# Optimization experiments

Hardware: AMD Instinct MI355X
Metric: run time of the kernel (lower is better)

## Reference

```python
import jax, jax.numpy as jnp
import numpy as np

N_CELL, N_NET, N_GCELL = 50000, 10000, 20000
E = 100000
D = 32   # hidden_node = hidden_net = hidden_hanna = out_node = out_net
DP = 16  # hidden_pin = hidden_edge feats


def setup_inputs() -> dict:
    key = jax.random.key(0)
    ks = jax.random.split(key, 21)
    f = jax.random.normal
    ri = lambda k, n: jax.random.randint(k, (E,), 0, n, dtype=jnp.int32)
    return {
        'node_feat': f(ks[0], (N_CELL, D), jnp.float32),
        'net_feat': f(ks[1], (N_NET, D), jnp.float32),
        'pin_feat': f(ks[2], (E, DP), jnp.float32),
        'hanna_feat': f(ks[3], (N_GCELL, D), jnp.float32),
        'edge_feat': f(ks[4], (E, DP), jnp.float32),
        'pins_src': ri(ks[5], N_CELL), 'pins_dst': ri(ks[6], N_NET),
        'pinned_src': ri(ks[7], N_NET), 'pinned_dst': ri(ks[8], N_CELL),
        'connect_src': ri(ks[9], N_GCELL), 'connect_dst': ri(ks[10], N_GCELL),
        'pt_src': ri(ks[11], N_CELL), 'pt_dst': ri(ks[12], N_GCELL),
        'pf_src': ri(ks[13], N_GCELL), 'pf_dst': ri(ks[14], N_CELL),
        'W_net': f(ks[15], (D, D)) * 0.1, 'b_net': jnp.zeros((D,), jnp.float32),
        'W_topo': f(ks[16], (DP, D * D)) * 0.1, 'b_topo': jnp.zeros((D * D,), jnp.float32),
        'W_pins': f(ks[17], (D, D)) * 0.1, 'b_pins': jnp.zeros((D,), jnp.float32),
        'W_connect': f(ks[18], (D, D)) * 0.1, 'b_connect': jnp.zeros((D,), jnp.float32),
        'W_pt': f(ks[19], (D, D)) * 0.1, 'b_pt': jnp.zeros((D,), jnp.float32),
        'b_pinned': jnp.zeros((D,), jnp.float32), 'b_pf': jnp.zeros((D,), jnp.float32),
    }


def _deg(idx, n):
    # clamped degree, as DGL clamps to min 1
    return jnp.maximum(jax.ops.segment_sum(jnp.ones_like(idx, jnp.float32), idx, n), 1.0)


def graph_conv(h_src, W, b, src, dst, n_src, n_dst):
    # DGL GraphConv with norm='both': D_out^{-1/2} gather -> sum -> D_in^{-1/2}, then W, b
    feat = (h_src * _deg(src, n_src)[:, None] ** -0.5) @ W
    agg = jax.ops.segment_sum(feat[src], dst, n_dst)
    return agg * _deg(dst, n_dst)[:, None] ** -0.5 + b


def nn_conv(h_src, efeat, W_topo, b_topo, bias, src, dst, n_dst):
    # DGL NNConv (aggregator='mean'): per-edge weight from edge_func, mean over in-edges
    d_in = h_src.shape[1]
    w = (efeat @ W_topo + b_topo).reshape(-1, d_in, bias.shape[0])  # (E, d_in, d_out)
    m = jnp.einsum('ei,eio->eo', h_src[src], w)
    return jax.ops.segment_sum(m, dst, n_dst) / _deg(dst, n_dst)[:, None] + bias


def reference(node_feat, net_feat, pin_feat, hanna_feat, edge_feat,
              pins_src, pins_dst, pinned_src, pinned_dst, connect_src, connect_dst,
              pt_src, pt_dst, pf_src, pf_dst,
              W_net, b_net, W_topo, b_topo, W_pins, b_pins,
              W_connect, b_connect, W_pt, b_pt, b_pinned, b_pf):
    # 'pins': cell -> net (GraphConv)
    h_net = graph_conv(node_feat, W_pins, b_pins, pins_src, pins_dst, N_CELL, N_NET)
    # 'pinned': net -> cell (NNConv) + 'point-from': gcell -> cell (NNConv); agg='sum'
    h_cell = (nn_conv(net_feat, pin_feat, W_topo, b_topo, b_pinned, pinned_src, pinned_dst, N_CELL)
              + nn_conv(hanna_feat, edge_feat, W_topo, b_topo, b_pf, pf_src, pf_dst, N_CELL))
    # 'connect': gcell -> gcell + 'point-to': cell -> gcell (GraphConvs); agg='sum'
    h_gcell = (graph_conv(hanna_feat, W_connect, b_connect, connect_src, connect_dst, N_GCELL, N_GCELL)
               + graph_conv(node_feat, W_pt, b_pt, pt_src, pt_dst, N_CELL, N_GCELL))
    return (h_cell, h_net + net_feat @ W_net + b_net, h_gcell)
```

## Files before the change

kernel.cpp:

```cpp
#include <hip/hip_runtime.h>

typedef unsigned short u16;
typedef unsigned int u32;

#define NC 50000
#define NN 10000
#define NG 20000
#define NE 100000
#define NSCAN 150016
#define NBLK 74


__device__ __forceinline__ float bflo(u32 a) { return __uint_as_float(a << 16); }
__device__ __forceinline__ float bfhi(u32 a) { return __uint_as_float(a & 0xFFFF0000u); }
__device__ __forceinline__ u16 fbf(float f) {
  u32 u = __float_as_uint(f);
  return (u16)((u + 0x7FFFu + ((u >> 16) & 1u)) >> 16);
}

__device__ __forceinline__ float nn_msg(int e, int s, const float* __restrict__ ef,
                                        const u16* __restrict__ T,
                                        const float* __restrict__ C, int o) {
  const float4* efp = reinterpret_cast<const float4*>(ef + (size_t)e * 16);
  float4 ea = efp[0], eb = efp[1], ec = efp[2], ed = efp[3];
  const uint4* tp = reinterpret_cast<const uint4*>(T + (size_t)s * 512 + o * 16);
  uint4 ta = tp[0], tb = tp[1];
  float m = C[(size_t)s * 32 + o];
  m += ea.x * bflo(ta.x) + ea.y * bfhi(ta.x) + ea.z * bflo(ta.y) + ea.w * bfhi(ta.y);
  m += eb.x * bflo(ta.z) + eb.y * bfhi(ta.z) + eb.z * bflo(ta.w) + eb.w * bfhi(ta.w);
  m += ec.x * bflo(tb.x) + ec.y * bfhi(tb.x) + ec.z * bflo(tb.y) + ec.w * bfhi(tb.y);
  m += ed.x * bflo(tb.z) + ed.y * bfhi(tb.z) + ed.z * bflo(tb.w) + ed.w * bfhi(tb.w);
  return m;
}

__global__ __launch_bounds__(512) void k_front(
    const float* __restrict__ feat_net, const float* __restrict__ feat_han,
    const float* __restrict__ W_topo, const float* __restrict__ b_topo,
    u16* __restrict__ T_net, u16* __restrict__ T_han,
    float* __restrict__ C_net, float* __restrict__ C_han,
    const int* __restrict__ pins_src, const int* __restrict__ pins_dst,
    const int* __restrict__ pinned_dst, const int* __restrict__ pf_dst,
    const int* __restrict__ connect_src, const int* __restrict__ connect_dst,
    const int* __restrict__ pt_src, const int* __restrict__ pt_dst,
    int* __restrict__ hist, int* __restrict__ srccnt) {
  int b = blockIdx.x;
  int tid = threadIdx.x;
  if (b < 469) {
    __shared__ float hs[64][32];
    int nd0 = b * 64;
    {
      int idx = tid * 4;
      int nl = idx >> 5, i = idx & 31;
      int ng = nd0 + nl;
      int ngc = min(ng, 29999);
      const float* rp = (ngc < NN) ? feat_net + (size_t)ngc * 32
                                   : feat_han + (size_t)(ngc - NN) * 32;
      *reinterpret_cast<float4*>(&hs[nl][i]) =
          *reinterpret_cast<const float4*>(rp + i);
    }
    int jj = tid & 255;
    int j0 = jj * 2, j1 = j0 + 1;
    int p0 = j0 & 15, o0 = j0 >> 4;
    int p1 = j1 & 15, o1 = j1 >> 4;
    float w0[32], w1[32];
#pragma unroll
    for (int i = 0; i < 32; i++) {
      w0[i] = W_topo[p0 * 1024 + i * 32 + o0];
      w1[i] = W_topo[p1 * 1024 + i * 32 + o1];
    }
    __syncthreads();
    int g = tid >> 8;
#pragma unroll 4
    for (int n = 0; n < 32; n++) {
      int nl = g * 32 + n;
      float a0 = 0.f, a1 = 0.f;
#pragma unroll
      for (int i = 0; i < 32; i++) {
        float h = hs[nl][i];
        a0 += h * w0[i];
        a1 += h * w1[i];
      }
      int s = nd0 + nl;
      if (s < 30000) {
        u32 pk = (u32)fbf(a0) | ((u32)fbf(a1) << 16);
        u32* dst = (s < NN)
            ? reinterpret_cast<u32*>(T_net + (size_t)s * 512 + j0)
            : reinterpret_cast<u32*>(T_han + (size_t)(s - NN) * 512 + j0);
        *dst = pk;
      }
    }
    return;
  }
  if (b < 2344) {
    int t = (b - 469) * 512 + tid;
    int s2 = t >> 5, o = t & 31;
    bool han = s2 >= NN;
    const float* feat = han ? feat_han : feat_net;
    float* C = han ? C_han : C_net;
    int s = han ? s2 - NN : s2;
    float acc = 0.f;
#pragma unroll 8
    for (int i = 0; i < 32; i++)
      acc += feat[(size_t)s * 32 + i] * b_topo[i * 32 + o];
    C[(size_t)s * 32 + o] = acc;
    return;
  }
  int e = (b - 2344) * 512 + tid;
  if (e >= NE) return;
  atomicAdd(&hist[pins_dst[e]], 1);
  atomicAdd(&hist[10000 + connect_dst[e]], 1);
  atomicAdd(&hist[30000 + pt_dst[e]], 1);
  atomicAdd(&hist[50000 + pinned_dst[e]], 1);
  atomicAdd(&hist[100000 + pf_dst[e]], 1);
  atomicAdd(&srccnt[pins_src[e]], 1);
  atomicAdd(&srccnt[50000 + connect_src[e]], 1);
  atomicAdd(&srccnt[70000 + pt_src[e]], 1);
}

__global__ __launch_bounds__(256) void k_scan1(
    const int* __restrict__ cnt, int* __restrict__ bsum) {
  __shared__ int sm[256];
  int b = blockIdx.x, tid = threadIdx.x;
  int base = b * 2048 + tid * 8;
  int tot = 0;
#pragma unroll
  for (int j = 0; j < 8; j++) {
    int i = base + j;
    tot += (i < NSCAN) ? cnt[i] : 0;
  }
  sm[tid] = tot;
  __syncthreads();
  for (int off = 128; off > 0; off >>= 1) {
    if (tid < off) sm[tid] += sm[tid + off];
    __syncthreads();
  }
  if (tid == 0) bsum[b] = sm[0];
}

__global__ __launch_bounds__(256) void k_scan3(
    const int* __restrict__ cnt, const int* __restrict__ bsum,
    int* __restrict__ bases) {
  __shared__ int sm[256];
  __shared__ int carry;
  int b = blockIdx.x, tid = threadIdx.x;
  if (tid == 0) {
    int run = 0;
    for (int i = 0; i < b; i++) run += bsum[i];
    carry = run;
  }
  int base = b * 2048 + tid * 8;
  int v[8];
  int tot = 0;
#pragma unroll
  for (int j = 0; j < 8; j++) {
    int i = base + j;
    v[j] = (i < NSCAN) ? cnt[i] : 0;
    tot += v[j];
  }
  sm[tid] = tot;
  __syncthreads();
  for (int off = 1; off < 256; off <<= 1) {
    int add = (tid >= off) ? sm[tid - off] : 0;
    __syncthreads();
    sm[tid] += add;
    __syncthreads();
  }
  int excl = sm[tid] - tot + carry;
#pragma unroll
  for (int j = 0; j < 8; j++) {
    int i = base + j;
    if (i < NSCAN) bases[i] = excl;
    excl += v[j];
  }
}

__global__ __launch_bounds__(512) void k_fill(
    const int* __restrict__ pins_src, const int* __restrict__ pins_dst,
    const int* __restrict__ connect_src, const int* __restrict__ connect_dst,
    const int* __restrict__ pt_src, const int* __restrict__ pt_dst,
    const int* __restrict__ pinned_src, const int* __restrict__ pinned_dst,
    const int* __restrict__ pf_src, const int* __restrict__ pf_dst,
    const int* __restrict__ srccnt,
    const int* __restrict__ bases, int* __restrict__ cursor,
    int2* __restrict__ csr_gc, int2* __restrict__ csr_nn) {
  int t = blockIdx.x * 512 + threadIdx.x;
  if (t >= 5 * NE) return;
  int r = (t >= NE) + (t >= 2 * NE) + (t >= 3 * NE) + (t >= 4 * NE);
  int e = t - r * NE;
  const int* srcs = r == 0 ? pins_src : r == 1 ? connect_src
                   : r == 2 ? pt_src : r == 3 ? pinned_src : pf_src;
  const int* dsts = r == 0 ? pins_dst : r == 1 ? connect_dst
                   : r == 2 ? pt_dst : r == 3 ? pinned_dst : pf_dst;
  int off = r == 0 ? 0 : r == 1 ? 10000 : r == 2 ? 30000 : r == 3 ? 50000 : 100000;
  int s = srcs[e];
  int g = off + dsts[e];
  int pos = atomicAdd(&cursor[g], 1);
  int cpos = bases[g] + pos;
  if (r < 3) {
    int soff = r == 0 ? 0 : r == 1 ? 50000 : 70000;
    float w = rsqrtf(fmaxf((float)srccnt[soff + s], 1.f));
    csr_gc[cpos] = make_int2(s, __float_as_int(w));
  } else {
    csr_nn[cpos - 300000] = make_int2(e, s);
  }
}

__global__ __launch_bounds__(512) void k_gc_gather(
    const int* __restrict__ hist, const int* __restrict__ bases,
    const int2* __restrict__ csr_gc,
    const float* __restrict__ node_feat, const float* __restrict__ hanna_feat,
    float* __restrict__ S_net, float* __restrict__ S_conn, float* __restrict__ S_pt) {
  int t = blockIdx.x * 512 + threadIdx.x;
  int rr = t >> 5, o = t & 31;
  int rel = (rr >= 10000) + (rr >= 30000);
  const float* feat = (rel == 1) ? hanna_feat : node_feat;
  float* S = rel == 0 ? S_net + (size_t)rr * 32
           : rel == 1 ? S_conn + (size_t)(rr - 10000) * 32
                      : S_pt + (size_t)(rr - 30000) * 32;
  int base = bases[rr], deg = hist[rr];
  float acc = 0.f;
  int k = 0;
  for (; k + 1 < deg; k += 2) {
    int2 pa = csr_gc[base + k], pb = csr_gc[base + k + 1];
    acc += feat[(size_t)pa.x * 32 + o] * __int_as_float(pa.y) +
           feat[(size_t)pb.x * 32 + o] * __int_as_float(pb.y);
  }
  if (k < deg) {
    int2 pa = csr_gc[base + k];
    acc += feat[(size_t)pa.x * 32 + o] * __int_as_float(pa.y);
  }
  S[o] = acc;
}

__global__ __launch_bounds__(512) void k_tail(
    const int* __restrict__ hist, const int* __restrict__ bases,
    const int2* __restrict__ csr_nn,
    const float* __restrict__ pin_feat, const float* __restrict__ edge_feat,
    const u16* __restrict__ T_net, const u16* __restrict__ T_han,
    const float* __restrict__ C_net, const float* __restrict__ C_han,
    const float* __restrict__ b_pinned, const float* __restrict__ b_pf,
    const float* __restrict__ S_net, const float* __restrict__ net_feat,
    const float* __restrict__ W_pins, const float* __restrict__ b_pins,
    const float* __restrict__ W_net, const float* __restrict__ b_net,
    const float* __restrict__ S_conn, const float* __restrict__ S_pt,
    const float* __restrict__ W_connect, const float* __restrict__ b_connect,
    const float* __restrict__ W_pt, const float* __restrict__ b_pt,
    float* __restrict__ out) {
  __shared__ float Wa[1024], Wb[1024];
  int b = blockIdx.x;
  if (b < 3125) {
    int t = b * 512 + threadIdx.x;
    int d = t >> 5, o = t & 31;
    float a0 = 0.f, a1 = 0.f;
    {
      int g = 50000 + d;
      int base = bases[g] - 300000, deg = hist[g];
      int k = 0;
      for (; k + 1 < deg; k += 2) {
        int2 ea = csr_nn[base + k], eb = csr_nn[base + k + 1];
        a0 += nn_msg(ea.x, ea.y, pin_feat, T_net, C_net, o) +
              nn_msg(eb.x, eb.y, pin_feat, T_net, C_net, o);
      }
      if (k < deg) {
        int2 ea = csr_nn[base + k];
        a0 += nn_msg(ea.x, ea.y, pin_feat, T_net, C_net, o);
      }
      a0 /= fmaxf((float)deg, 1.f);
    }
    {
      int g = 100000 + d;
      int base = bases[g] - 300000, deg = hist[g];
      int k = 0;
      for (; k + 1 < deg; k += 2) {
        int2 ea = csr_nn[base + k], eb = csr_nn[base + k + 1];
        a1 += nn_msg(ea.x, ea.y, edge_feat, T_han, C_han, o) +
              nn_msg(eb.x, eb.y, edge_feat, T_han, C_han, o);
      }
      if (k < deg) {
        int2 ea = csr_nn[base + k];
        a1 += nn_msg(ea.x, ea.y, edge_feat, T_han, C_han, o);
      }
      a1 /= fmaxf((float)deg, 1.f);
    }
    out[(size_t)d * 32 + o] = a0 + a1 + b_pinned[o] + b_pf[o];
    return;
  }
  if (b < 3750) {
    for (int k = threadIdx.x; k < 1024; k += 512) {
      Wa[k] = W_pins[k];
      Wb[k] = W_net[k];
    }
    __syncthreads();
    int t = (b - 3125) * 512 + threadIdx.x;
    int r = t >> 5, o = t & 31;
    float a1 = 0.f, a2 = 0.f;
#pragma unroll 8
    for (int i = 0; i < 32; i++) {
      a1 += S_net[(size_t)r * 32 + i] * Wa[i * 32 + o];
      a2 += net_feat[(size_t)r * 32 + i] * Wb[i * 32 + o];
    }
    out[1600000 + t] = a1 * rsqrtf(fmaxf((float)hist[r], 1.f)) + b_pins[o] +
                       a2 + b_net[o];
    return;
  }
  for (int k = threadIdx.x; k < 1024; k += 512) {
    Wa[k] = W_connect[k];
    Wb[k] = W_pt[k];
  }
  __syncthreads();
  int t = (b - 3750) * 512 + threadIdx.x;
  int r = t >> 5, o = t & 31;
  float a1 = 0.f, a2 = 0.f;
#pragma unroll 8
  for (int i = 0; i < 32; i++) {
    a1 += S_conn[(size_t)r * 32 + i] * Wa[i * 32 + o];
    a2 += S_pt[(size_t)r * 32 + i] * Wb[i * 32 + o];
  }
  out[1920000 + t] = a1 * rsqrtf(fmaxf((float)hist[10000 + r], 1.f)) + b_connect[o] +
                     a2 * rsqrtf(fmaxf((float)hist[30000 + r], 1.f)) + b_pt[o];
}

extern "C" void kernel_launch(void* const* d_in, const int* in_sizes, int n_in,
                              void* d_out, int out_size, void* d_ws, size_t ws_size,
                              hipStream_t stream) {
  const float* node_feat  = (const float*)d_in[0];
  const float* net_feat   = (const float*)d_in[1];
  const float* pin_feat   = (const float*)d_in[2];
  const float* hanna_feat = (const float*)d_in[3];
  const float* edge_feat  = (const float*)d_in[4];
  const int* pins_src    = (const int*)d_in[5];
  const int* pins_dst    = (const int*)d_in[6];
  const int* pinned_src  = (const int*)d_in[7];
  const int* pinned_dst  = (const int*)d_in[8];
  const int* connect_src = (const int*)d_in[9];
  const int* connect_dst = (const int*)d_in[10];
  const int* pt_src      = (const int*)d_in[11];
  const int* pt_dst      = (const int*)d_in[12];
  const int* pf_src      = (const int*)d_in[13];
  const int* pf_dst      = (const int*)d_in[14];
  const float* W_net     = (const float*)d_in[15];
  const float* b_net     = (const float*)d_in[16];
  const float* W_topo    = (const float*)d_in[17];
  const float* b_topo    = (const float*)d_in[18];
  const float* W_pins    = (const float*)d_in[19];
  const float* b_pins    = (const float*)d_in[20];
  const float* W_connect = (const float*)d_in[21];
  const float* b_connect = (const float*)d_in[22];
  const float* W_pt      = (const float*)d_in[23];
  const float* b_pt      = (const float*)d_in[24];
  const float* b_pinned  = (const float*)d_in[25];
  const float* b_pf      = (const float*)d_in[26];
  float* out = (float*)d_out;

  int* wi = (int*)d_ws;
  int* hist    = wi + 0;
  int* cursor  = wi + 150016;
  int* srccnt  = wi + 300032;
  int* bases   = wi + 420032;
  int* bsum    = wi + 570064;
  int2* csr_gc = (int2*)(wi + 570192);
  int2* csr_nn = (int2*)(wi + 1170192);
  float* wf = (float*)d_ws;
  float* S_net  = wf + 1570192;
  float* S_conn = wf + 1890192;
  float* S_pt   = wf + 2530192;
  float* C_net  = wf + 3170192;
  float* C_han  = wf + 3490192;
  u16* T_net = (u16*)((char*)d_ws + 16520832);
  u16* T_han = (u16*)((char*)d_ws + 16520832 + 10240000);

  hipMemsetAsync(d_ws, 0, 420032 * sizeof(int), stream);

  k_front<<<2540, 512, 0, stream>>>(
      net_feat, hanna_feat, W_topo, b_topo, T_net, T_han, C_net, C_han,
      pins_src, pins_dst, pinned_dst, pf_dst, connect_src, connect_dst,
      pt_src, pt_dst, hist, srccnt);

  k_scan1<<<NBLK, 256, 0, stream>>>(hist, bsum);
  k_scan3<<<NBLK, 256, 0, stream>>>(hist, bsum, bases);

  k_fill<<<(5 * NE + 511) / 512, 512, 0, stream>>>(
      pins_src, pins_dst, connect_src, connect_dst, pt_src, pt_dst,
      pinned_src, pinned_dst, pf_src, pf_dst, srccnt, bases, cursor,
      csr_gc, csr_nn);

  k_gc_gather<<<3125, 512, 0, stream>>>(
      hist, bases, csr_gc, node_feat, hanna_feat, S_net, S_conn, S_pt);

  k_tail<<<5000, 512, 0, stream>>>(
      hist, bases, csr_nn, pin_feat, edge_feat,
      T_net, T_han, C_net, C_han, b_pinned, b_pf,
      S_net, net_feat, W_pins, b_pins, W_net, b_net,
      S_conn, S_pt, W_connect, b_connect, W_pt, b_pt, out);
}
```

Before: 283.6 us.

## Fuse GraphConv gather with projection, merge scan kernels, widen topo register tile

The GraphConv gather kernel now applies the W_pins/W_net and W_connect/W_pt projections directly from shared memory, so the S_net/S_conn/S_pt intermediates are no longer written to and reread from global memory. The tail kernel keeps only the NNConv aggregation. The two-pass scan becomes one kernel in which each block recomputes its prefix by summing all earlier counts. The front kernel computes four outputs per thread with float4 shared loads, which uses more registers. The trade-offs are one fewer launch and less global traffic, against redundant prefix reads in the scan and higher register pressure.

```diff
diff --git a/kernel.cpp b/kernel.cpp
--- a/kernel.cpp
+++ b/kernel.cpp
@@ -51,42 +51,43 @@
     {
       int idx = tid * 4;
       int nl = idx >> 5, i = idx & 31;
-      int ng = nd0 + nl;
-      int ngc = min(ng, 29999);
-      const float* rp = (ngc < NN) ? feat_net + (size_t)ngc * 32
-                                   : feat_han + (size_t)(ngc - NN) * 32;
+      int ng = min(nd0 + nl, 29999);
+      const float* rp = (ng < NN) ? feat_net + (size_t)ng * 32
+                                  : feat_han + (size_t)(ng - NN) * 32;
       *reinterpret_cast<float4*>(&hs[nl][i]) =
           *reinterpret_cast<const float4*>(rp + i);
     }
-    int jj = tid & 255;
-    int j0 = jj * 2, j1 = j0 + 1;
-    int p0 = j0 & 15, o0 = j0 >> 4;
-    int p1 = j1 & 15, o1 = j1 >> 4;
-    float w0[32], w1[32];
+    int jj = tid & 127, grp = tid >> 7;
+    int j0 = jj * 4;
+    int o = j0 >> 4, p0 = j0 & 15;
+    float w0[32], w1[32], w2[32], w3[32];
 #pragma unroll
     for (int i = 0; i < 32; i++) {
-      w0[i] = W_topo[p0 * 1024 + i * 32 + o0];
-      w1[i] = W_topo[p1 * 1024 + i * 32 + o1];
-    }
-    __syncthreads();
-    int g = tid >> 8;
-#pragma unroll 4
-    for (int n = 0; n < 32; n++) {
-      int nl = g * 32 + n;
-      float a0 = 0.f, a1 = 0.f;
+      w0[i] = W_topo[(p0 + 0) * 1024 + i * 32 + o];
+      w1[i] = W_topo[(p0 + 1) * 1024 + i * 32 + o];
+      w2[i] = W_topo[(p0 + 2) * 1024 + i * 32 + o];
+      w3[i] = W_topo[(p0 + 3) * 1024 + i * 32 + o];
+    }
+    __syncthreads();
+#pragma unroll 2
+    for (int n = 0; n < 16; n++) {
+      int nl = grp * 16 + n;
+      float a0 = 0.f, a1 = 0.f, a2 = 0.f, a3 = 0.f;
 #pragma unroll
-      for (int i = 0; i < 32; i++) {
-        float h = hs[nl][i];
-        a0 += h * w0[i];
-        a1 += h * w1[i];
+      for (int i4 = 0; i4 < 32; i4 += 4) {
+        float4 h = *reinterpret_cast<float4*>(&hs[nl][i4]);
+        a0 += h.x * w0[i4] + h.y * w0[i4 + 1] + h.z * w0[i4 + 2] + h.w * w0[i4 + 3];
+        a1 += h.x * w1[i4] + h.y * w1[i4 + 1] + h.z * w1[i4 + 2] + h.w * w1[i4 + 3];
+        a2 += h.x * w2[i4] + h.y * w2[i4 + 1] + h.z * w2[i4 + 2] + h.w * w2[i4 + 3];
+        a3 += h.x * w3[i4] + h.y * w3[i4 + 1] + h.z * w3[i4 + 2] + h.w * w3[i4 + 3];
       }
       int s = nd0 + nl;
       if (s < 30000) {
-        u32 pk = (u32)fbf(a0) | ((u32)fbf(a1) << 16);
-        u32* dst = (s < NN)
-            ? reinterpret_cast<u32*>(T_net + (size_t)s * 512 + j0)
-            : reinterpret_cast<u32*>(T_han + (size_t)(s - NN) * 512 + j0);
-        *dst = pk;
+        uint2 pk = make_uint2((u32)fbf(a0) | ((u32)fbf(a1) << 16),
+                              (u32)fbf(a2) | ((u32)fbf(a3) << 16));
+        u16* tb = (s < NN) ? T_net + (size_t)s * 512 + j0
+                           : T_han + (size_t)(s - NN) * 512 + j0;
+        *reinterpret_cast<uint2*>(tb) = pk;
       }
     }
     return;
@@ -117,37 +118,25 @@
   atomicAdd(&srccnt[70000 + pt_src[e]], 1);
 }
 
-__global__ __launch_bounds__(256) void k_scan1(
-    const int* __restrict__ cnt, int* __restrict__ bsum) {
+__global__ __launch_bounds__(256) void k_scan(
+    const int* __restrict__ cnt, int* __restrict__ bases) {
   __shared__ int sm[256];
+  __shared__ int carryS;
   int b = blockIdx.x, tid = threadIdx.x;
-  int base = b * 2048 + tid * 8;
-  int tot = 0;
-#pragma unroll
-  for (int j = 0; j < 8; j++) {
-    int i = base + j;
-    tot += (i < NSCAN) ? cnt[i] : 0;
-  }
-  sm[tid] = tot;
+  int lim = b * 2048;
+  int part = 0;
+  for (int i = tid * 4; i < lim; i += 1024) {
+    int4 v = *reinterpret_cast<const int4*>(cnt + i);
+    part += v.x + v.y + v.z + v.w;
+  }
+  sm[tid] = part;
   __syncthreads();
   for (int off = 128; off > 0; off >>= 1) {
     if (tid < off) sm[tid] += sm[tid + off];
     __syncthreads();
   }
-  if (tid == 0) bsum[b] = sm[0];
-}
-
-__global__ __launch_bounds__(256) void k_scan3(
-    const int* __restrict__ cnt, const int* __restrict__ bsum,
-    int* __restrict__ bases) {
-  __shared__ int sm[256];
-  __shared__ int carry;
-  int b = blockIdx.x, tid = threadIdx.x;
-  if (tid == 0) {
-    int run = 0;
-    for (int i = 0; i < b; i++) run += bsum[i];
-    carry = run;
-  }
+  if (tid == 0) carryS = sm[0];
+  __syncthreads();
   int base = b * 2048 + tid * 8;
   int v[8];
   int tot = 0;
@@ -165,7 +154,7 @@
     sm[tid] += add;
     __syncthreads();
   }
-  int excl = sm[tid] - tot + carry;
+  int excl = sm[tid] - tot + carryS;
 #pragma unroll
   for (int j = 0; j < 8; j++) {
     int i = base + j;
@@ -205,19 +194,62 @@
   }
 }
 
-__global__ __launch_bounds__(512) void k_gc_gather(
+__global__ __launch_bounds__(512) void k_gc_fin(
     const int* __restrict__ hist, const int* __restrict__ bases,
     const int2* __restrict__ csr_gc,
     const float* __restrict__ node_feat, const float* __restrict__ hanna_feat,
-    float* __restrict__ S_net, float* __restrict__ S_conn, float* __restrict__ S_pt) {
-  int t = blockIdx.x * 512 + threadIdx.x;
-  int rr = t >> 5, o = t & 31;
-  int rel = (rr >= 10000) + (rr >= 30000);
-  const float* feat = (rel == 1) ? hanna_feat : node_feat;
-  float* S = rel == 0 ? S_net + (size_t)rr * 32
-           : rel == 1 ? S_conn + (size_t)(rr - 10000) * 32
-                      : S_pt + (size_t)(rr - 30000) * 32;
-  int base = bases[rr], deg = hist[rr];
+    const float* __restrict__ net_feat,
+    const float* __restrict__ W_pins, const float* __restrict__ b_pins,
+    const float* __restrict__ W_net, const float* __restrict__ b_net,
+    const float* __restrict__ W_connect, const float* __restrict__ b_connect,
+    const float* __restrict__ W_pt, const float* __restrict__ b_pt,
+    float* __restrict__ out) {
+  __shared__ float Wa[1024], Wb[1024];
+  __shared__ float srow[16][32];
+  int b = blockIdx.x, tid = threadIdx.x;
+  if (b < 625) {
+    for (int k = tid; k < 1024; k += 512) {
+      Wa[k] = W_pins[k];
+      Wb[k] = W_net[k];
+    }
+    int rl = tid >> 5, o = tid & 31;
+    int r = b * 16 + rl;
+    int base = bases[r], deg = hist[r];
+    float acc = 0.f;
+    int k = 0;
+    for (; k + 1 < deg; k += 2) {
+      int2 pa = csr_gc[base + k], pb = csr_gc[base + k + 1];
+      acc += node_feat[(size_t)pa.x * 32 + o] * __int_as_float(pa.y) +
+             node_feat[(size_t)pb.x * 32 + o] * __int_as_float(pb.y);
+    }
+    if (k < deg) {
+      int2 pa = csr_gc[base + k];
+      acc += node_feat[(size_t)pa.x * 32 + o] * __int_as_float(pa.y);
+    }
+    srow[rl][o] = acc;
+    __syncthreads();
+    float a1 = 0.f, a2 = 0.f;
+#pragma unroll 8
+    for (int i = 0; i < 32; i++) {
+      a1 += srow[rl][i] * Wa[i * 32 + o];
+      a2 += net_feat[(size_t)r * 32 + i] * Wb[i * 32 + o];
+    }
+    out[1600000 + (size_t)r * 32 + o] =
+        a1 * rsqrtf(fmaxf((float)deg, 1.f)) + b_pins[o] + a2 + b_net[o];
+    return;
+  }
+  int bb = b - 625;
+  for (int k = tid; k < 1024; k += 512) {
+    Wa[k] = W_connect[k];
+    Wb[k] = W_pt[k];
+  }
+  int rl = tid >> 6;
+  int half = (tid >> 5) & 1;
+  int o = tid & 31;
+  int r = bb * 8 + rl;
+  int g = (half ? 30000 : 10000) + r;
+  const float* feat = half ? node_feat : hanna_feat;
+  int base = bases[g], deg = hist[g];
   float acc = 0.f;
   int k = 0;
   for (; k + 1 < deg; k += 2) {
@@ -229,7 +261,19 @@
     int2 pa = csr_gc[base + k];
     acc += feat[(size_t)pa.x * 32 + o] * __int_as_float(pa.y);
   }
-  S[o] = acc;
+  srow[rl * 2 + half][o] = acc;
+  __syncthreads();
+  if (half == 0) {
+    float a1 = 0.f, a2 = 0.f;
+#pragma unroll 8
+    for (int i = 0; i < 32; i++) {
+      a1 += srow[rl * 2 + 0][i] * Wa[i * 32 + o];
+      a2 += srow[rl * 2 + 1][i] * Wb[i * 32 + o];
+    }
+    out[1920000 + (size_t)r * 32 + o] =
+        a1 * rsqrtf(fmaxf((float)hist[10000 + r], 1.f)) + b_connect[o] +
+        a2 * rsqrtf(fmaxf((float)hist[30000 + r], 1.f)) + b_pt[o];
+  }
 }
 
 __global__ __launch_bounds__(512) void k_tail(
@@ -239,85 +283,41 @@
     const u16* __restrict__ T_net, const u16* __restrict__ T_han,
     const float* __restrict__ C_net, const float* __restrict__ C_han,
     const float* __restrict__ b_pinned, const float* __restrict__ b_pf,
-    const float* __restrict__ S_net, const float* __restrict__ net_feat,
-    const float* __restrict__ W_pins, const float* __restrict__ b_pins,
-    const float* __restrict__ W_net, const float* __restrict__ b_net,
-    const float* __restrict__ S_conn, const float* __restrict__ S_pt,
-    const float* __restrict__ W_connect, const float* __restrict__ b_connect,
-    const float* __restrict__ W_pt, const float* __restrict__ b_pt,
     float* __restrict__ out) {
-  __shared__ float Wa[1024], Wb[1024];
-  int b = blockIdx.x;
-  if (b < 3125) {
-    int t = b * 512 + threadIdx.x;
-    int d = t >> 5, o = t & 31;
-    float a0 = 0.f, a1 = 0.f;
-    {
-      int g = 50000 + d;
-      int base = bases[g] - 300000, deg = hist[g];
-      int k = 0;
-      for (; k + 1 < deg; k += 2) {
-        int2 ea = csr_nn[base + k], eb = csr_nn[base + k + 1];
-        a0 += nn_msg(ea.x, ea.y, pin_feat, T_net, C_net, o) +
-              nn_msg(eb.x, eb.y, pin_feat, T_net, C_net, o);
-      }
-      if (k < deg) {
-        int2 ea = csr_nn[base + k];
-        a0 += nn_msg(ea.x, ea.y, pin_feat, T_net, C_net, o);
-      }
-      a0 /= fmaxf((float)deg, 1.f);
-    }
-    {
-      int g = 100000 + d;
-      int base = bases[g] - 300000, deg = hist[g];
-      int k = 0;
-      for (; k + 1 < deg; k += 2) {
-        int2 ea = csr_nn[base + k], eb = csr_nn[base + k + 1];
-        a1 += nn_msg(ea.x, ea.y, edge_feat, T_han, C_han, o) +
-              nn_msg(eb.x, eb.y, edge_feat, T_han, C_han, o);
-      }
-      if (k < deg) {
-        int2 ea = csr_nn[base + k];
-        a1 += nn_msg(ea.x, ea.y, edge_feat, T_han, C_han, o);
-      }
-      a1 /= fmaxf((float)deg, 1.f);
-    }
-    out[(size_t)d * 32 + o] = a0 + a1 + b_pinned[o] + b_pf[o];
-    return;
-  }
-  if (b < 3750) {
-    for (int k = threadIdx.x; k < 1024; k += 512) {
-      Wa[k] = W_pins[k];
-      Wb[k] = W_net[k];
-    }
-    __syncthreads();
-    int t = (b - 3125) * 512 + threadIdx.x;
-    int r = t >> 5, o = t & 31;
-    float a1 = 0.f, a2 = 0.f;
-#pragma unroll 8
-    for (int i = 0; i < 32; i++) {
-      a1 += S_net[(size_t)r * 32 + i] * Wa[i * 32 + o];
-      a2 += net_feat[(size_t)r * 32 + i] * Wb[i * 32 + o];
-    }
-    out[1600000 + t] = a1 * rsqrtf(fmaxf((float)hist[r], 1.f)) + b_pins[o] +
-                       a2 + b_net[o];
-    return;
-  }
-  for (int k = threadIdx.x; k < 1024; k += 512) {
-    Wa[k] = W_connect[k];
-    Wb[k] = W_pt[k];
-  }
-  __syncthreads();
-  int t = (b - 3750) * 512 + threadIdx.x;
-  int r = t >> 5, o = t & 31;
-  float a1 = 0.f, a2 = 0.f;
-#pragma unroll 8
-  for (int i = 0; i < 32; i++) {
-    a1 += S_conn[(size_t)r * 32 + i] * Wa[i * 32 + o];
-    a2 += S_pt[(size_t)r * 32 + i] * Wb[i * 32 + o];
-  }
-  out[1920000 + t] = a1 * rsqrtf(fmaxf((float)hist[10000 + r], 1.f)) + b_connect[o] +
-                     a2 * rsqrtf(fmaxf((float)hist[30000 + r], 1.f)) + b_pt[o];
+  int t = blockIdx.x * 512 + threadIdx.x;
+  int d = t >> 5, o = t & 31;
+  float a0 = 0.f, a1 = 0.f;
+  {
+    int g = 50000 + d;
+    int base = bases[g] - 300000, deg = hist[g];
+    int k = 0;
+    for (; k + 1 < deg; k += 2) {
+      int2 ea = csr_nn[base + k], eb = csr_nn[base + k + 1];
+      a0 += nn_msg(ea.x, ea.y, pin_feat, T_net, C_net, o) +
+            nn_msg(eb.x, eb.y, pin_feat, T_net, C_net, o);
+    }
+    if (k < deg) {
+      int2 ea = csr_nn[base + k];
+      a0 += nn_msg(ea.x, ea.y, pin_feat, T_net, C_net, o);
+    }
+    a0 /= fmaxf((float)deg, 1.f);
+  }
+  {
+    int g = 100000 + d;
+    int base = bases[g] - 300000, deg = hist[g];
+    int k = 0;
+    for (; k + 1 < deg; k += 2) {
+      int2 ea = csr_nn[base + k], eb = csr_nn[base + k + 1];
+      a1 += nn_msg(ea.x, ea.y, edge_feat, T_han, C_han, o) +
+            nn_msg(eb.x, eb.y, edge_feat, T_han, C_han, o);
+    }
+    if (k < deg) {
+      int2 ea = csr_nn[base + k];
+      a1 += nn_msg(ea.x, ea.y, edge_feat, T_han, C_han, o);
+    }
+    a1 /= fmaxf((float)deg, 1.f);
+  }
+  out[(size_t)d * 32 + o] = a0 + a1 + b_pinned[o] + b_pf[o];
 }
 
 extern "C" void kernel_launch(void* const* d_in, const int* in_sizes, int n_in,
@@ -357,17 +357,13 @@
   int* cursor  = wi + 150016;
   int* srccnt  = wi + 300032;
   int* bases   = wi + 420032;
-  int* bsum    = wi + 570064;
   int2* csr_gc = (int2*)(wi + 570192);
   int2* csr_nn = (int2*)(wi + 1170192);
   float* wf = (float*)d_ws;
-  float* S_net  = wf + 1570192;
-  float* S_conn = wf + 1890192;
-  float* S_pt   = wf + 2530192;
-  float* C_net  = wf + 3170192;
-  float* C_han  = wf + 3490192;
-  u16* T_net = (u16*)((char*)d_ws + 16520832);
-  u16* T_han = (u16*)((char*)d_ws + 16520832 + 10240000);
+  float* C_net  = wf + 1570192;
+  float* C_han  = wf + 1890192;
+  u16* T_net = (u16*)((char*)d_ws + 10120832);
+  u16* T_han = (u16*)((char*)d_ws + 10120832 + 10240000);
 
   hipMemsetAsync(d_ws, 0, 420032 * sizeof(int), stream);
 
@@ -376,20 +372,18 @@
       pins_src, pins_dst, pinned_dst, pf_dst, connect_src, connect_dst,
       pt_src, pt_dst, hist, srccnt);
 
-  k_scan1<<<NBLK, 256, 0, stream>>>(hist, bsum);
-  k_scan3<<<NBLK, 256, 0, stream>>>(hist, bsum, bases);
+  k_scan<<<NBLK, 256, 0, stream>>>(hist, bases);
 
   k_fill<<<(5 * NE + 511) / 512, 512, 0, stream>>>(
       pins_src, pins_dst, connect_src, connect_dst, pt_src, pt_dst,
       pinned_src, pinned_dst, pf_src, pf_dst, srccnt, bases, cursor,
       csr_gc, csr_nn);
 
-  k_gc_gather<<<3125, 512, 0, stream>>>(
-      hist, bases, csr_gc, node_feat, hanna_feat, S_net, S_conn, S_pt);
-
-  k_tail<<<5000, 512, 0, stream>>>(
+  k_gc_fin<<<3125, 512, 0, stream>>>(
+      hist, bases, csr_gc, node_feat, hanna_feat, net_feat,
+      W_pins, b_pins, W_net, b_net, W_connect, b_connect, W_pt, b_pt, out);
+
+  k_tail<<<3125, 512, 0, stream>>>(
       hist, bases, csr_nn, pin_feat, edge_feat,
-      T_net, T_han, C_net, C_han, b_pinned, b_pf,
-      S_net, net_feat, W_pins, b_pins, W_net, b_net,
-      S_conn, S_pt, W_connect, b_connect, W_pt, b_pt, out);
-}
+      T_net, T_han, C_net, C_han, b_pinned, b_pf, out);
+}
```

Result: slower. 311.4 us (+9.8%).

## Restructure per-node W_topo transform blocks and merge two-pass scan into one kernel

Applied to the files above, without the earlier changes.

The T-table projection in k_front now assigns one output column per thread over 32 nodes per block, giving 938 blocks instead of 469 with 64 nodes each and two columns per thread. It stages 4 nodes at a time in shared memory with a sync per group and writes 16-bit values instead of packed 32-bit pairs. The two-kernel block scan is replaced by a single kernel in which each block recomputes its prefix carry by summing all earlier counts itself. This removes one launch and the bsum round trip, but adds redundant reads that grow with block index and more barriers in the transform loop.

```diff
diff --git a/kernel.cpp b/kernel.cpp
--- a/kernel.cpp
+++ b/kernel.cpp
@@ -45,54 +45,42 @@
     int* __restrict__ hist, int* __restrict__ srccnt) {
   int b = blockIdx.x;
   int tid = threadIdx.x;
-  if (b < 469) {
-    __shared__ float hs[64][32];
-    int nd0 = b * 64;
-    {
-      int idx = tid * 4;
-      int nl = idx >> 5, i = idx & 31;
-      int ng = nd0 + nl;
-      int ngc = min(ng, 29999);
-      const float* rp = (ngc < NN) ? feat_net + (size_t)ngc * 32
-                                   : feat_han + (size_t)(ngc - NN) * 32;
-      *reinterpret_cast<float4*>(&hs[nl][i]) =
-          *reinterpret_cast<const float4*>(rp + i);
-    }
-    int jj = tid & 255;
-    int j0 = jj * 2, j1 = j0 + 1;
-    int p0 = j0 & 15, o0 = j0 >> 4;
-    int p1 = j1 & 15, o1 = j1 >> 4;
-    float w0[32], w1[32];
-#pragma unroll
-    for (int i = 0; i < 32; i++) {
-      w0[i] = W_topo[p0 * 1024 + i * 32 + o0];
-      w1[i] = W_topo[p1 * 1024 + i * 32 + o1];
-    }
-    __syncthreads();
-    int g = tid >> 8;
-#pragma unroll 4
-    for (int n = 0; n < 32; n++) {
-      int nl = g * 32 + n;
-      float a0 = 0.f, a1 = 0.f;
-#pragma unroll
-      for (int i = 0; i < 32; i++) {
-        float h = hs[nl][i];
-        a0 += h * w0[i];
-        a1 += h * w1[i];
-      }
-      int s = nd0 + nl;
-      if (s < 30000) {
-        u32 pk = (u32)fbf(a0) | ((u32)fbf(a1) << 16);
-        u32* dst = (s < NN)
-            ? reinterpret_cast<u32*>(T_net + (size_t)s * 512 + j0)
-            : reinterpret_cast<u32*>(T_han + (size_t)(s - NN) * 512 + j0);
-        *dst = pk;
+  if (b < 938) {
+    __shared__ float hs[4][32];
+    bool han = b >= 313;
+    const float* feat = han ? feat_han : feat_net;
+    u16* T = han ? T_han : T_net;
+    int n = han ? NG : NN;
+    int blk = han ? (b - 313) : b;
+    int j = tid;
+    int p = j & 15, o = j >> 4;
+    float w[32];
+#pragma unroll
+    for (int i = 0; i < 32; i++) w[i] = W_topo[p * 1024 + i * 32 + o];
+    int s0 = blk * 32;
+    int s1 = min(s0 + 32, n);
+    for (int s = s0; s < s1; s += 4) {
+      __syncthreads();
+      if (tid < 128) {
+        int r = tid >> 5, i = tid & 31;
+        int sn = s + r;
+        hs[r][i] = (sn < s1) ? feat[(size_t)sn * 32 + i] : 0.f;
+      }
+      __syncthreads();
+#pragma unroll
+      for (int r = 0; r < 4; r++) {
+        int sn = s + r;
+        if (sn >= s1) break;
+        float acc = 0.f;
+#pragma unroll
+        for (int i = 0; i < 32; i++) acc += hs[r][i] * w[i];
+        T[(size_t)sn * 512 + j] = fbf(acc);
       }
     }
     return;
   }
-  if (b < 2344) {
-    int t = (b - 469) * 512 + tid;
+  if (b < 2813) {
+    int t = (b - 938) * 512 + tid;
     int s2 = t >> 5, o = t & 31;
     bool han = s2 >= NN;
     const float* feat = han ? feat_han : feat_net;
@@ -105,7 +93,7 @@
     C[(size_t)s * 32 + o] = acc;
     return;
   }
-  int e = (b - 2344) * 512 + tid;
+  int e = (b - 2813) * 512 + tid;
   if (e >= NE) return;
   atomicAdd(&hist[pins_dst[e]], 1);
   atomicAdd(&hist[10000 + connect_dst[e]], 1);
@@ -117,37 +105,25 @@
   atomicAdd(&srccnt[70000 + pt_src[e]], 1);
 }
 
-__global__ __launch_bounds__(256) void k_scan1(
-    const int* __restrict__ cnt, int* __restrict__ bsum) {
+__global__ __launch_bounds__(256) void k_scan(
+    const int* __restrict__ cnt, int* __restrict__ bases) {
   __shared__ int sm[256];
+  __shared__ int carryS;
   int b = blockIdx.x, tid = threadIdx.x;
-  int base = b * 2048 + tid * 8;
-  int tot = 0;
-#pragma unroll
-  for (int j = 0; j < 8; j++) {
-    int i = base + j;
-    tot += (i < NSCAN) ? cnt[i] : 0;
-  }
-  sm[tid] = tot;
+  int lim = b * 2048;
+  int part = 0;
+  for (int i = tid * 4; i < lim; i += 1024) {
+    int4 v = *reinterpret_cast<const int4*>(cnt + i);
+    part += v.x + v.y + v.z + v.w;
+  }
+  sm[tid] = part;
   __syncthreads();
   for (int off = 128; off > 0; off >>= 1) {
     if (tid < off) sm[tid] += sm[tid + off];
     __syncthreads();
   }
-  if (tid == 0) bsum[b] = sm[0];
-}
-
-__global__ __launch_bounds__(256) void k_scan3(
-    const int* __restrict__ cnt, const int* __restrict__ bsum,
-    int* __restrict__ bases) {
-  __shared__ int sm[256];
-  __shared__ int carry;
-  int b = blockIdx.x, tid = threadIdx.x;
-  if (tid == 0) {
-    int run = 0;
-    for (int i = 0; i < b; i++) run += bsum[i];
-    carry = run;
-  }
+  if (tid == 0) carryS = sm[0];
+  __syncthreads();
   int base = b * 2048 + tid * 8;
   int v[8];
   int tot = 0;
@@ -165,7 +141,7 @@
     sm[tid] += add;
     __syncthreads();
   }
-  int excl = sm[tid] - tot + carry;
+  int excl = sm[tid] - tot + carryS;
 #pragma unroll
   for (int j = 0; j < 8; j++) {
     int i = base + j;
@@ -357,7 +333,6 @@
   int* cursor  = wi + 150016;
   int* srccnt  = wi + 300032;
   int* bases   = wi + 420032;
-  int* bsum    = wi + 570064;
   int2* csr_gc = (int2*)(wi + 570192);
   int2* csr_nn = (int2*)(wi + 1170192);
   float* wf = (float*)d_ws;
@@ -371,13 +346,12 @@
 
   hipMemsetAsync(d_ws, 0, 420032 * sizeof(int), stream);
 
-  k_front<<<2540, 512, 0, stream>>>(
+  k_front<<<3009, 512, 0, stream>>>(
       net_feat, hanna_feat, W_topo, b_topo, T_net, T_han, C_net, C_han,
       pins_src, pins_dst, pinned_dst, pf_dst, connect_src, connect_dst,
       pt_src, pt_dst, hist, srccnt);
 
-  k_scan1<<<NBLK, 256, 0, stream>>>(hist, bsum);
-  k_scan3<<<NBLK, 256, 0, stream>>>(hist, bsum, bases);
+  k_scan<<<NBLK, 256, 0, stream>>>(hist, bases);
 
   k_fill<<<(5 * NE + 511) / 512, 512, 0, stream>>>(
       pins_src, pins_dst, connect_src, connect_dst, pt_src, pt_dst,
```

After: 314.7 us. 1.11x slower.
